# Performance work log

Hardware: AMD Instinct MI355X
Metric: run time of the kernel (lower is better)

Reference implementation:

```python
import jax, jax.numpy as jnp
import numpy as np

B, C, H, W = 8, 256, 64, 64
NUM_HEADS = 4


def setup_inputs() -> dict:
    key = jax.random.key(0)
    ks = jax.random.split(key, 6)
    s = 0.02  # small init scale for 1x1 conv weights
    return {
        "x": jax.random.normal(ks[0], (B, C, H, W), jnp.float32),
        "cproj": jax.random.normal(ks[1], (B, C, H, W), jnp.float32),
        "wq": jax.random.normal(ks[2], (C, C), jnp.float32) * s,
        "bq": jnp.zeros((C,), jnp.float32),
        "wkv": jax.random.normal(ks[3], (2 * C, C), jnp.float32) * s,
        "bkv": jnp.zeros((2 * C,), jnp.float32),
        "wo": jax.random.normal(ks[4], (C, C), jnp.float32) * s,  # zero_module in torch; random here for a meaningful baseline
        "bo": jnp.zeros((C,), jnp.float32),
    }


def reference(x, cproj, wq, bq, wkv, bkv, wo, bo):
    Bb, Cc, Hh, Ww = x.shape
    N = Hh * Ww
    h = NUM_HEADS
    d = Cc // h
    scale = 1.0 / jnp.sqrt(jnp.sqrt(jnp.asarray(Cc, jnp.float32)))

    xf = x.reshape(Bb, Cc, N)
    cf = cproj.reshape(Bb, Cc, N)

    # 1x1 convs == channel matmuls
    Q = jnp.einsum('oc,bcn->bon', wq, xf) + bq[None, :, None]           # (B,C,N)
    KV = jnp.einsum('oc,bcn->bon', wkv, cf) + bkv[None, :, None]        # (B,2C,N)
    K, V = KV[:, :Cc], KV[:, Cc:]

    # softmax over channel-dim-within-head for q, over spatial N for k
    q = jax.nn.softmax(Q.reshape(Bb, h, d, N) * scale, axis=2).reshape(Bb, Cc, N)
    k = jax.nn.softmax(K.reshape(Bb, h, d, N), axis=3).reshape(Bb, Cc, N)

    # linear-attention: (B,C,C) context, then project back to N — note heads are mixed, per original bmm
    context = jnp.einsum('bcn,bdn->bcd', k, V)
    out = jnp.einsum('bcd,bdn->bcn', context, q)

    out = jnp.einsum('oc,bcn->bon', wo, out) + bo[None, :, None]
    return out.reshape(Bb, Cc, Hh, Ww)
```

## Files before the change

kernel.cpp:

```cpp
#include <hip/hip_runtime.h>

#define B_ 8
#define C_ 256
#define N_ 4096
#define NSPLIT 16

typedef float f32x4 __attribute__((ext_vector_type(4)));
typedef __bf16 bf16x8 __attribute__((ext_vector_type(8)));
typedef unsigned short u16x8 __attribute__((ext_vector_type(8)));
typedef unsigned short u16x4 __attribute__((ext_vector_type(4)));

__device__ __forceinline__ unsigned short f2bf(float f) {
  unsigned u = __float_as_uint(f);
  u += 0x7fff + ((u >> 16) & 1);
  return (unsigned short)(u >> 16);
}

__device__ __forceinline__ f32x4 mfma16(bf16x8 a, bf16x8 b, f32x4 c) {
  return __builtin_amdgcn_mfma_f32_16x16x32_bf16(a, b, c, 0, 0, 0);
}

typedef __attribute__((address_space(1))) const void* gvp;
typedef __attribute__((address_space(3))) void* lvp;
__device__ __forceinline__ void gld16(const void* g, void* l) {
  __builtin_amdgcn_global_load_lds((gvp)g, (lvp)l, 16, 0, 0);
}

template <int ROWS>
__device__ __forceinline__ void stage(unsigned short* lds, const unsigned short* g,
                                      int ld, int w, int lane) {
  const int r8 = lane >> 3;
  const int ce = ((lane & 7) ^ r8) << 3;
  const unsigned short* gp = g + (size_t)(w * (ROWS / 4) + r8) * ld + ce;
  unsigned short* lp = lds + w * (ROWS / 4) * 64;
#pragma unroll
  for (int i = 0; i < ROWS / 32; i++)
    gld16(gp + (size_t)(i * 8) * ld, lp + i * 512);
}

__device__ __forceinline__ bf16x8 frag(const unsigned short* lds, int row, int kc) {
  return *(const bf16x8*)(lds + row * 64 + ((kc ^ (row & 7)) << 3));
}

__device__ __forceinline__ void loadB(float4* pbv, const float* src, int ld,
                                      int n0, int kt, int w, int lane) {
  const int nf = lane & 15, kg = lane >> 4;
  const float* sp = src + (size_t)(kt * 64 + w * 16 + kg * 4) * ld + n0 + 4 * nf;
#pragma unroll
  for (int i = 0; i < 4; i++) pbv[i] = *(const float4*)(sp + (size_t)i * ld);
}
__device__ __forceinline__ void writeB(unsigned short* Bs, const float4* pbv,
                                       int w, int lane) {
  const int nf = lane & 15, kg = lane >> 4;
  const int k0 = w * 16 + kg * 4;
#pragma unroll
  for (int j = 0; j < 4; j++) {
    u16x4 o = (u16x4){f2bf(((const float*)&pbv[0])[j]), f2bf(((const float*)&pbv[1])[j]),
                      f2bf(((const float*)&pbv[2])[j]), f2bf(((const float*)&pbv[3])[j])};
    *(u16x4*)&Bs[(4 * nf + j) * 68 + k0] = o;
  }
}
__device__ __forceinline__ bf16x8 fragB(const unsigned short* Bs, int n, int k8) {
  union { u16x4 q[2]; bf16x8 b; } u;
  const unsigned short* p = Bs + n * 68 + k8 * 8;
  u.q[0] = *(const u16x4*)p;
  u.q[1] = *(const u16x4*)(p + 4);
  return u.b;
}

__device__ __forceinline__ bf16x8 fragC(const unsigned short* Ct, int n, int k8) {
  union { u16x4 q[2]; bf16x8 b; } u;
  const unsigned short* p = Ct + n * 268 + k8 * 8;
  u.q[0] = *(const u16x4*)p;
  u.q[1] = *(const u16x4*)(p + 4);
  return u.b;
}

__global__ __launch_bounds__(256) void castw(
    const float* __restrict__ wq, const float* __restrict__ wkv,
    const float* __restrict__ wo, unsigned short* __restrict__ wqb,
    unsigned short* __restrict__ wkvb, unsigned short* __restrict__ wob,
    float* __restrict__ Z) {
  int t = blockIdx.x * 256 + threadIdx.x;
  if (t < B_ * C_) Z[t] = 0.f;
  int i = t * 4;
  const float* src;
  unsigned short* dst;
  int off;
  if (i < 65536) { src = wq; dst = wqb; off = i; }
  else if (i < 196608) { src = wkv; dst = wkvb; off = i - 65536; }
  else { src = wo; dst = wob; off = i - 196608; }
  float4 v = *(const float4*)(src + off);
  *(u16x4*)(dst + off) = (u16x4){f2bf(v.x), f2bf(v.y), f2bf(v.z), f2bf(v.w)};
}

__device__ __forceinline__ void qproj_body(
    unsigned short* As, unsigned short* Bs, const unsigned short* __restrict__ wqb,
    const float* __restrict__ x, const float* __restrict__ bq,
    unsigned short* __restrict__ qT, int b, int n0, int m0b) {
  const int tid = threadIdx.x, lane = tid & 63, w = tid >> 6;
  const int m0w = (w >> 1) * 64;
  const int n0w = (w & 1) * 32;
  const int colL = lane & 15, kq = lane >> 4, quad = lane >> 4;
  const float* xb = x + (size_t)b * C_ * N_;

  f32x4 acc[4][2];
#pragma unroll
  for (int i = 0; i < 4; i++)
#pragma unroll
    for (int j = 0; j < 2; j++) acc[i][j] = (f32x4){0.f, 0.f, 0.f, 0.f};

  float4 pbv[4];
  loadB(pbv, xb, N_, n0, 0, w, lane);

  for (int kt = 0; kt < 4; kt++) {
    writeB(Bs, pbv, w, lane);
    stage<128>(As, wqb + (size_t)m0b * C_ + kt * 64, C_, w, lane);
    __syncthreads();
    if (kt < 3) loadB(pbv, xb, N_, n0, kt + 1, w, lane);
#pragma unroll
    for (int ks = 0; ks < 2; ks++) {
      bf16x8 af[4], bf[2];
#pragma unroll
      for (int mt = 0; mt < 4; mt++) af[mt] = frag(As, m0w + mt * 16 + colL, ks * 4 + kq);
#pragma unroll
      for (int nt = 0; nt < 2; nt++) bf[nt] = fragB(Bs, n0w + nt * 16 + colL, ks * 4 + kq);
#pragma unroll
      for (int mt = 0; mt < 4; mt++)
#pragma unroll
        for (int nt = 0; nt < 2; nt++) acc[mt][nt] = mfma16(af[mt], bf[nt], acc[mt][nt]);
    }
    __syncthreads();
  }

#pragma unroll
  for (int nt = 0; nt < 2; nt++) {
    float v[16];
    float mx = -1e30f;
#pragma unroll
    for (int mt = 0; mt < 4; mt++)
#pragma unroll
      for (int r = 0; r < 4; r++) {
        int m = m0b + m0w + mt * 16 + quad * 4 + r;
        float val = (acc[mt][nt][r] + bq[m]) * 0.25f;
        v[mt * 4 + r] = val;
        mx = fmaxf(mx, val);
      }
    mx = fmaxf(mx, __shfl_xor(mx, 16));
    mx = fmaxf(mx, __shfl_xor(mx, 32));
    float s = 0.f;
#pragma unroll
    for (int j = 0; j < 16; j++) { v[j] = __expf(v[j] - mx); s += v[j]; }
    s += __shfl_xor(s, 16);
    s += __shfl_xor(s, 32);
    float inv = 1.0f / s;
    const int n = n0 + n0w + nt * 16 + colL;
    unsigned short* qb = qT + ((size_t)b * N_ + n) * C_ + m0b + m0w;
#pragma unroll
    for (int mt = 0; mt < 4; mt++) {
      u16x4 o = (u16x4){f2bf(v[mt * 4 + 0] * inv), f2bf(v[mt * 4 + 1] * inv),
                        f2bf(v[mt * 4 + 2] * inv), f2bf(v[mt * 4 + 3] * inv)};
      *(u16x4*)(qb + mt * 16 + quad * 4) = o;
    }
  }
}

__device__ __forceinline__ void kvproj_body(
    unsigned short* As, unsigned short* Bs, const unsigned short* __restrict__ wkvb,
    const float* __restrict__ cp, const float* __restrict__ bkv,
    float* __restrict__ Kf, unsigned short* __restrict__ Vb,
    float* __restrict__ Z, int b, int n0, int m0b) {
  const int tid = threadIdx.x, lane = tid & 63, w = tid >> 6;
  const int m0w = w * 32;
  const int colL = lane & 15, kq = lane >> 4, quad = lane >> 4;
  const float* cpb = cp + (size_t)b * C_ * N_;

  f32x4 acc[2][4];
#pragma unroll
  for (int i = 0; i < 2; i++)
#pragma unroll
    for (int j = 0; j < 4; j++) acc[i][j] = (f32x4){0.f, 0.f, 0.f, 0.f};

  float4 pbv[4];
  loadB(pbv, cpb, N_, n0, 0, w, lane);

  for (int kt = 0; kt < 4; kt++) {
    writeB(Bs, pbv, w, lane);
    stage<128>(As, wkvb + (size_t)m0b * C_ + kt * 64, C_, w, lane);
    __syncthreads();
    if (kt < 3) loadB(pbv, cpb, N_, n0, kt + 1, w, lane);
#pragma unroll
    for (int ks = 0; ks < 2; ks++) {
      bf16x8 bf[4];
#pragma unroll
      for (int nt = 0; nt < 4; nt++) bf[nt] = fragB(Bs, nt * 16 + colL, ks * 4 + kq);
#pragma unroll
      for (int mt = 0; mt < 2; mt++) {
        bf16x8 af = frag(As, m0w + mt * 16 + colL, ks * 4 + kq);
#pragma unroll
        for (int nt = 0; nt < 4; nt++) acc[mt][nt] = mfma16(af, bf[nt], acc[mt][nt]);
      }
    }
    __syncthreads();
  }

#pragma unroll
  for (int mt = 0; mt < 2; mt++)
#pragma unroll
    for (int r = 0; r < 4; r++) {
      int m = m0b + m0w + mt * 16 + quad * 4 + r;
      float bias = bkv[m];
      if (m < C_) {
        float* kr = Kf + ((size_t)b * C_ + m) * N_ + n0;
        float es = 0.f;
#pragma unroll
        for (int nt = 0; nt < 4; nt++) {
          float vv = acc[mt][nt][r] + bias;
          kr[nt * 16 + colL] = vv;
          es += __expf(vv);
        }
        es += __shfl_xor(es, 1);
        es += __shfl_xor(es, 2);
        es += __shfl_xor(es, 4);
        es += __shfl_xor(es, 8);
        if ((lane & 15) == 0) atomicAdd(&Z[b * C_ + m], es);
      } else {
        unsigned short* vr = Vb + ((size_t)b * C_ + m - C_) * N_ + n0;
#pragma unroll
        for (int nt = 0; nt < 4; nt++) vr[nt * 16 + colL] = f2bf(acc[mt][nt][r] + bias);
      }
    }
}

__global__ __launch_bounds__(256) void qkvproj(
    const unsigned short* __restrict__ wqb, const unsigned short* __restrict__ wkvb,
    const float* __restrict__ x, const float* __restrict__ cp,
    const float* __restrict__ bq, const float* __restrict__ bkv,
    unsigned short* __restrict__ qT, float* __restrict__ Kf,
    unsigned short* __restrict__ Vb, float* __restrict__ Z) {
  __shared__ __align__(16) unsigned short As[128 * 64];
  __shared__ __align__(16) unsigned short Bs[64 * 68];
  const int b = blockIdx.z, n0 = blockIdx.x * 64;
  if (blockIdx.y < 2)
    qproj_body(As, Bs, wqb, x, bq, qT, b, n0, blockIdx.y * 128);
  else
    kvproj_body(As, Bs, wkvb, cp, bkv, Kf, Vb, Z, b, n0, (blockIdx.y - 2) * 128);
}

__global__ __launch_bounds__(256) void ctx_part(
    const float* __restrict__ Kf, const float* __restrict__ Z,
    const unsigned short* __restrict__ Vb, float* __restrict__ ctxp) {
  __shared__ __align__(16) unsigned short As[128 * 64];
  __shared__ __align__(16) unsigned short Bs[64 * 64];
  const int z = blockIdx.z, b = z >> 4, s = z & 15;
  const int m0 = blockIdx.y * 128, n0 = blockIdx.x * 64;
  const int tid = threadIdx.x, lane = tid & 63, w = tid >> 6;
  const int m0w = (w & 1) * 64, n0w = (w >> 1) * 32;
  const int colL = lane & 15, kq = lane >> 4, quad = lane >> 4;
  const int kbeg = s * (N_ / NSPLIT);

  const int arow = tid >> 1, ahalf = tid & 1;
  const float* akf = Kf + ((size_t)b * C_ + m0 + arow) * N_ + kbeg + ahalf * 32;
  const float invz = 1.0f / Z[b * C_ + m0 + arow];
  const unsigned short* Bg = Vb + ((size_t)b * C_ + n0) * N_ + kbeg;

  f32x4 acc[4][2];
#pragma unroll
  for (int i = 0; i < 4; i++)
#pragma unroll
    for (int j = 0; j < 2; j++) acc[i][j] = (f32x4){0.f, 0.f, 0.f, 0.f};

  for (int kt = 0; kt < (N_ / NSPLIT) / 64; kt++) {
    stage<64>(Bs, Bg + kt * 64, N_, w, lane);
#pragma unroll
    for (int j = 0; j < 4; j++) {
      float4 a0 = *(const float4*)(akf + kt * 64 + j * 8);
      float4 a1 = *(const float4*)(akf + kt * 64 + j * 8 + 4);
      const int c8 = ahalf * 4 + j;
      u16x8 o = (u16x8){f2bf(__expf(a0.x) * invz), f2bf(__expf(a0.y) * invz),
                        f2bf(__expf(a0.z) * invz), f2bf(__expf(a0.w) * invz),
                        f2bf(__expf(a1.x) * invz), f2bf(__expf(a1.y) * invz),
                        f2bf(__expf(a1.z) * invz), f2bf(__expf(a1.w) * invz)};
      *(u16x8*)&As[arow * 64 + ((c8 ^ (arow & 7)) << 3)] = o;
    }
    __syncthreads();
#pragma unroll
    for (int ks = 0; ks < 2; ks++) {
      bf16x8 af[4], bf[2];
#pragma unroll
      for (int mt = 0; mt < 4; mt++) af[mt] = frag(As, m0w + mt * 16 + colL, ks * 4 + kq);
#pragma unroll
      for (int nt = 0; nt < 2; nt++) bf[nt] = frag(Bs, n0w + nt * 16 + colL, ks * 4 + kq);
#pragma unroll
      for (int mt = 0; mt < 4; mt++)
#pragma unroll
        for (int nt = 0; nt < 2; nt++) acc[mt][nt] = mfma16(af[mt], bf[nt], acc[mt][nt]);
    }
    __syncthreads();
  }

  float* outp = ctxp + ((size_t)s * B_ + b) * C_ * C_;
#pragma unroll
  for (int mt = 0; mt < 4; mt++)
#pragma unroll
    for (int nt = 0; nt < 2; nt++)
#pragma unroll
      for (int r = 0; r < 4; r++) {
        int m = m0 + m0w + mt * 16 + quad * 4 + r;
        int n = n0 + n0w + nt * 16 + colL;
        outp[(size_t)m * C_ + n] = acc[mt][nt][r];
      }
}

__global__ __launch_bounds__(256) void ctxoproj(
    const float* __restrict__ ctxp, const unsigned short* __restrict__ wob,
    unsigned short* __restrict__ ctx2) {
  __shared__ __align__(16) unsigned short AsW[4 * 64 * 64];
  __shared__ __align__(16) unsigned short Ct[32 * 268];
  const int b = blockIdx.z, o0 = blockIdx.y * 64, d0 = blockIdx.x * 32;
  const int tid = threadIdx.x, lane = tid & 63, w = tid >> 6;
  const int colL = lane & 15, kq = lane >> 4, quad = lane >> 4;

#pragma unroll
  for (int ck = 0; ck < 4; ck++)
    stage<64>(AsW + ck * 4096, wob + (size_t)o0 * C_ + ck * 64, C_, w, lane);

  const int q = tid & 7, cl = tid >> 3;
  const float* pb = ctxp + ((size_t)b * C_ + cl) * C_ + d0 + q * 4;
#pragma unroll 2
  for (int p = 0; p < 8; p++) {
    f32x4 s4 = (f32x4){0.f, 0.f, 0.f, 0.f};
    const float* pp = pb + (size_t)p * 32 * C_;
#pragma unroll
    for (int s = 0; s < NSPLIT; s++) {
      float4 v = *(const float4*)(pp + (size_t)s * B_ * C_ * C_);
      s4[0] += v.x; s4[1] += v.y; s4[2] += v.z; s4[3] += v.w;
    }
    const int c = p * 32 + cl;
#pragma unroll
    for (int j = 0; j < 4; j++) Ct[(q * 4 + j) * 268 + c] = f2bf(s4[j]);
  }
  __syncthreads();

  f32x4 acc2[2];
  acc2[0] = (f32x4){0.f, 0.f, 0.f, 0.f};
  acc2[1] = (f32x4){0.f, 0.f, 0.f, 0.f};
#pragma unroll
  for (int kt = 0; kt < 4; kt++)
#pragma unroll
    for (int ks = 0; ks < 2; ks++) {
      bf16x8 af = frag(AsW + kt * 4096, w * 16 + colL, ks * 4 + kq);
#pragma unroll
      for (int nt = 0; nt < 2; nt++) {
        bf16x8 bf = fragC(Ct, nt * 16 + colL, kt * 8 + ks * 4 + kq);
        acc2[nt] = mfma16(af, bf, acc2[nt]);
      }
    }
  unsigned short* ob = ctx2 + (size_t)b * C_ * C_;
#pragma unroll
  for (int nt = 0; nt < 2; nt++)
#pragma unroll
    for (int r = 0; r < 4; r++)
      ob[(size_t)(o0 + w * 16 + quad * 4 + r) * C_ + d0 + nt * 16 + colL] =
          f2bf(acc2[nt][r]);
}

__global__ __launch_bounds__(256) void outgemm(
    const unsigned short* __restrict__ ctx2, const unsigned short* __restrict__ qT,
    const float* __restrict__ bo, float* __restrict__ out) {
  __shared__ __align__(16) unsigned short As[128 * 64];
  __shared__ __align__(16) unsigned short Bs[64 * 64];
  const int b = blockIdx.z, n0 = blockIdx.x * 64, m0b = blockIdx.y * 128;
  const int tid = threadIdx.x, lane = tid & 63, w = tid >> 6;
  const int m0w = w * 32;
  const int colL = lane & 15, kq = lane >> 4, quad = lane >> 4;
  const unsigned short* Ag = ctx2 + (size_t)b * C_ * C_ + (size_t)m0b * C_;
  const unsigned short* Bg = qT + ((size_t)b * N_ + n0) * C_;

  f32x4 acc[2][4];
#pragma unroll
  for (int i = 0; i < 2; i++)
#pragma unroll
    for (int j = 0; j < 4; j++) acc[i][j] = (f32x4){0.f, 0.f, 0.f, 0.f};

  for (int kt = 0; kt < 4; kt++) {
    stage<128>(As, Ag + kt * 64, C_, w, lane);
    stage<64>(Bs, Bg + kt * 64, C_, w, lane);
    __syncthreads();
#pragma unroll
    for (int ks = 0; ks < 2; ks++) {
      bf16x8 af[2], bf[4];
#pragma unroll
      for (int mt = 0; mt < 2; mt++) af[mt] = frag(As, m0w + mt * 16 + colL, ks * 4 + kq);
#pragma unroll
      for (int nt = 0; nt < 4; nt++) bf[nt] = frag(Bs, nt * 16 + colL, ks * 4 + kq);
#pragma unroll
      for (int mt = 0; mt < 2; mt++)
#pragma unroll
        for (int nt = 0; nt < 4; nt++) acc[mt][nt] = mfma16(af[mt], bf[nt], acc[mt][nt]);
    }
    __syncthreads();
  }

  float* ob = out + (size_t)b * C_ * N_;
#pragma unroll
  for (int mt = 0; mt < 2; mt++)
#pragma unroll
    for (int r = 0; r < 4; r++) {
      int m = m0b + m0w + mt * 16 + quad * 4 + r;
      float bias = bo[m];
#pragma unroll
      for (int nt = 0; nt < 4; nt++) {
        int n = n0 + nt * 16 + colL;
        ob[(size_t)m * N_ + n] = acc[mt][nt][r] + bias;
      }
    }
}

extern "C" void kernel_launch(void* const* d_in, const int* in_sizes, int n_in,
                              void* d_out, int out_size, void* d_ws, size_t ws_size,
                              hipStream_t stream) {
  const float* x     = (const float*)d_in[0];
  const float* cproj = (const float*)d_in[1];
  const float* wq    = (const float*)d_in[2];
  const float* bq    = (const float*)d_in[3];
  const float* wkv   = (const float*)d_in[4];
  const float* bkv   = (const float*)d_in[5];
  const float* wo    = (const float*)d_in[6];
  const float* bo    = (const float*)d_in[7];
  float* out = (float*)d_out;

  unsigned short* qT    = (unsigned short*)d_ws;
  float*          Kf    = (float*)(qT + 8388608);
  unsigned short* Vb    = (unsigned short*)(Kf + 8388608);
  float*          ctxp  = (float*)(Vb + 8388608);
  unsigned short* wqb   = (unsigned short*)(ctxp + 8388608);
  unsigned short* wkvb  = wqb + 65536;
  unsigned short* wob   = wkvb + 131072;
  unsigned short* ctx2  = wob + 65536;
  float*          Zbuf  = (float*)(ctx2 + 524288);

  castw<<<256, 256, 0, stream>>>(wq, wkv, wo, wqb, wkvb, wob, Zbuf);
  qkvproj<<<dim3(64, 6, 8), 256, 0, stream>>>(wqb, wkvb, x, cproj, bq, bkv,
                                              qT, Kf, Vb, Zbuf);
  ctx_part<<<dim3(4, 2, 128), 256, 0, stream>>>(Kf, Zbuf, Vb, ctxp);
  ctxoproj<<<dim3(8, 4, 8), 256, 0, stream>>>(ctxp, wob, ctx2);
  outgemm<<<dim3(64, 2, 8), 256, 0, stream>>>(ctx2, qT, bo, out);
}
```

Measured before the change: 212.0 us.

## Pre-transpose inputs to bf16 and store exp(K) as bf16 for async staging

Adds a prep pass that casts x and cproj to bf16 and transposes them to N-major, so the projection GEMMs can stage both operands with direct global-to-LDS loads instead of register load, convert and scatter. The K projection now writes exp(K) as bf16 rather than fp32 logits, and the 1/Z normalisation moves to the ctx_part epilogue, which removes per-element exp and conversion from the context GEMM's inner loop. In exchange there is an extra full read and write of both inputs in the prep kernel and more workspace. The bf16 rounding of exp values before normalisation may change accuracy slightly.

```diff
diff --git a/kernel.cpp b/kernel.cpp
--- a/kernel.cpp
+++ b/kernel.cpp
@@ -42,32 +42,6 @@
   return *(const bf16x8*)(lds + row * 64 + ((kc ^ (row & 7)) << 3));
 }
 
-__device__ __forceinline__ void loadB(float4* pbv, const float* src, int ld,
-                                      int n0, int kt, int w, int lane) {
-  const int nf = lane & 15, kg = lane >> 4;
-  const float* sp = src + (size_t)(kt * 64 + w * 16 + kg * 4) * ld + n0 + 4 * nf;
-#pragma unroll
-  for (int i = 0; i < 4; i++) pbv[i] = *(const float4*)(sp + (size_t)i * ld);
-}
-__device__ __forceinline__ void writeB(unsigned short* Bs, const float4* pbv,
-                                       int w, int lane) {
-  const int nf = lane & 15, kg = lane >> 4;
-  const int k0 = w * 16 + kg * 4;
-#pragma unroll
-  for (int j = 0; j < 4; j++) {
-    u16x4 o = (u16x4){f2bf(((const float*)&pbv[0])[j]), f2bf(((const float*)&pbv[1])[j]),
-                      f2bf(((const float*)&pbv[2])[j]), f2bf(((const float*)&pbv[3])[j])};
-    *(u16x4*)&Bs[(4 * nf + j) * 68 + k0] = o;
-  }
-}
-__device__ __forceinline__ bf16x8 fragB(const unsigned short* Bs, int n, int k8) {
-  union { u16x4 q[2]; bf16x8 b; } u;
-  const unsigned short* p = Bs + n * 68 + k8 * 8;
-  u.q[0] = *(const u16x4*)p;
-  u.q[1] = *(const u16x4*)(p + 4);
-  return u.b;
-}
-
 __device__ __forceinline__ bf16x8 fragC(const unsigned short* Ct, int n, int k8) {
   union { u16x4 q[2]; bf16x8 b; } u;
   const unsigned short* p = Ct + n * 268 + k8 * 8;
@@ -76,33 +50,62 @@
   return u.b;
 }
 
-__global__ __launch_bounds__(256) void castw(
+__global__ __launch_bounds__(256) void prep(
+    const float* __restrict__ x, const float* __restrict__ cp,
     const float* __restrict__ wq, const float* __restrict__ wkv,
-    const float* __restrict__ wo, unsigned short* __restrict__ wqb,
+    const float* __restrict__ wo, unsigned short* __restrict__ xT,
+    unsigned short* __restrict__ cpT, unsigned short* __restrict__ wqb,
     unsigned short* __restrict__ wkvb, unsigned short* __restrict__ wob,
     float* __restrict__ Z) {
-  int t = blockIdx.x * 256 + threadIdx.x;
-  if (t < B_ * C_) Z[t] = 0.f;
-  int i = t * 4;
-  const float* src;
-  unsigned short* dst;
-  int off;
-  if (i < 65536) { src = wq; dst = wqb; off = i; }
-  else if (i < 196608) { src = wkv; dst = wkvb; off = i - 65536; }
-  else { src = wo; dst = wob; off = i - 196608; }
-  float4 v = *(const float4*)(src + off);
-  *(u16x4*)(dst + off) = (u16x4){f2bf(v.x), f2bf(v.y), f2bf(v.z), f2bf(v.w)};
+  const int bid = blockIdx.x, tid = threadIdx.x;
+  if (bid < 4096) {
+    const int ct = bid & 3, nt = (bid >> 2) & 63, b = (bid >> 8) & 7, s = bid >> 11;
+    const float* src = (s ? cp : x) + (size_t)b * C_ * N_;
+    unsigned short* dst = (s ? cpT : xT) + (size_t)b * N_ * C_;
+    const int n0 = nt * 64, c0 = ct * 64;
+    __shared__ unsigned short t[64][68];
+    const int c = tid >> 2, nq = (tid & 3) * 16;
+    const float* sp = src + (size_t)(c0 + c) * N_ + n0 + nq;
+#pragma unroll
+    for (int j = 0; j < 4; j++) {
+      float4 v = *(const float4*)(sp + j * 4);
+      *(u16x4*)&t[c][nq + j * 4] = (u16x4){f2bf(v.x), f2bf(v.y), f2bf(v.z), f2bf(v.w)};
+    }
+    __syncthreads();
+    const int n = tid >> 2, cq = (tid & 3) * 16;
+    union { unsigned short s16[16]; u16x8 v8[2]; } o;
+#pragma unroll
+    for (int j = 0; j < 16; j++) o.s16[j] = t[cq + j][n];
+    unsigned short* dp = dst + (size_t)(n0 + n) * C_ + c0 + cq;
+    *(u16x8*)dp = o.v8[0];
+    *(u16x8*)(dp + 8) = o.v8[1];
+  } else {
+    if (bid == 4096) {
+#pragma unroll
+      for (int j = 0; j < 8; j++) Z[tid * 8 + j] = 0.f;
+    }
+    int i = ((bid - 4096) * 256 + tid) * 4;
+    const float* src;
+    unsigned short* dst;
+    int off;
+    if (i < 65536) { src = wq; dst = wqb; off = i; }
+    else if (i < 196608) { src = wkv; dst = wkvb; off = i - 65536; }
+    else { src = wo; dst = wob; off = i - 196608; }
+    float4 v = *(const float4*)(src + off);
+    *(u16x4*)(dst + off) = (u16x4){f2bf(v.x), f2bf(v.y), f2bf(v.z), f2bf(v.w)};
+  }
 }
 
 __device__ __forceinline__ void qproj_body(
     unsigned short* As, unsigned short* Bs, const unsigned short* __restrict__ wqb,
-    const float* __restrict__ x, const float* __restrict__ bq,
+    const unsigned short* __restrict__ xT, const float* __restrict__ bq,
     unsigned short* __restrict__ qT, int b, int n0, int m0b) {
   const int tid = threadIdx.x, lane = tid & 63, w = tid >> 6;
   const int m0w = (w >> 1) * 64;
   const int n0w = (w & 1) * 32;
   const int colL = lane & 15, kq = lane >> 4, quad = lane >> 4;
-  const float* xb = x + (size_t)b * C_ * N_;
+  const unsigned short* Ag = wqb + (size_t)m0b * C_;
+  const unsigned short* Bg = xT + ((size_t)b * N_ + n0) * C_;
 
   f32x4 acc[4][2];
 #pragma unroll
@@ -110,21 +113,17 @@
 #pragma unroll
     for (int j = 0; j < 2; j++) acc[i][j] = (f32x4){0.f, 0.f, 0.f, 0.f};
 
-  float4 pbv[4];
-  loadB(pbv, xb, N_, n0, 0, w, lane);
-
   for (int kt = 0; kt < 4; kt++) {
-    writeB(Bs, pbv, w, lane);
-    stage<128>(As, wqb + (size_t)m0b * C_ + kt * 64, C_, w, lane);
-    __syncthreads();
-    if (kt < 3) loadB(pbv, xb, N_, n0, kt + 1, w, lane);
+    stage<128>(As, Ag + kt * 64, C_, w, lane);
+    stage<64>(Bs, Bg + kt * 64, C_, w, lane);
+    __syncthreads();
 #pragma unroll
     for (int ks = 0; ks < 2; ks++) {
       bf16x8 af[4], bf[2];
 #pragma unroll
       for (int mt = 0; mt < 4; mt++) af[mt] = frag(As, m0w + mt * 16 + colL, ks * 4 + kq);
 #pragma unroll
-      for (int nt = 0; nt < 2; nt++) bf[nt] = fragB(Bs, n0w + nt * 16 + colL, ks * 4 + kq);
+      for (int nt = 0; nt < 2; nt++) bf[nt] = frag(Bs, n0w + nt * 16 + colL, ks * 4 + kq);
 #pragma unroll
       for (int mt = 0; mt < 4; mt++)
 #pragma unroll
@@ -167,13 +166,14 @@
 
 __device__ __forceinline__ void kvproj_body(
     unsigned short* As, unsigned short* Bs, const unsigned short* __restrict__ wkvb,
-    const float* __restrict__ cp, const float* __restrict__ bkv,
-    float* __restrict__ Kf, unsigned short* __restrict__ Vb,
+    const unsigned short* __restrict__ cpT, const float* __restrict__ bkv,
+    unsigned short* __restrict__ Eb, unsigned short* __restrict__ Vb,
     float* __restrict__ Z, int b, int n0, int m0b) {
   const int tid = threadIdx.x, lane = tid & 63, w = tid >> 6;
   const int m0w = w * 32;
   const int colL = lane & 15, kq = lane >> 4, quad = lane >> 4;
-  const float* cpb = cp + (size_t)b * C_ * N_;
+  const unsigned short* Ag = wkvb + (size_t)m0b * C_;
+  const unsigned short* Bg = cpT + ((size_t)b * N_ + n0) * C_;
 
   f32x4 acc[2][4];
 #pragma unroll
@@ -181,19 +181,15 @@
 #pragma unroll
     for (int j = 0; j < 4; j++) acc[i][j] = (f32x4){0.f, 0.f, 0.f, 0.f};
 
-  float4 pbv[4];
-  loadB(pbv, cpb, N_, n0, 0, w, lane);
-
   for (int kt = 0; kt < 4; kt++) {
-    writeB(Bs, pbv, w, lane);
-    stage<128>(As, wkvb + (size_t)m0b * C_ + kt * 64, C_, w, lane);
-    __syncthreads();
-    if (kt < 3) loadB(pbv, cpb, N_, n0, kt + 1, w, lane);
+    stage<128>(As, Ag + kt * 64, C_, w, lane);
+    stage<64>(Bs, Bg + kt * 64, C_, w, lane);
+    __syncthreads();
 #pragma unroll
     for (int ks = 0; ks < 2; ks++) {
       bf16x8 bf[4];
 #pragma unroll
-      for (int nt = 0; nt < 4; nt++) bf[nt] = fragB(Bs, nt * 16 + colL, ks * 4 + kq);
+      for (int nt = 0; nt < 4; nt++) bf[nt] = frag(Bs, nt * 16 + colL, ks * 4 + kq);
 #pragma unroll
       for (int mt = 0; mt < 2; mt++) {
         bf16x8 af = frag(As, m0w + mt * 16 + colL, ks * 4 + kq);
@@ -211,13 +207,13 @@
       int m = m0b + m0w + mt * 16 + quad * 4 + r;
       float bias = bkv[m];
       if (m < C_) {
-        float* kr = Kf + ((size_t)b * C_ + m) * N_ + n0;
+        unsigned short* er = Eb + ((size_t)b * C_ + m) * N_ + n0;
         float es = 0.f;
 #pragma unroll
         for (int nt = 0; nt < 4; nt++) {
-          float vv = acc[mt][nt][r] + bias;
-          kr[nt * 16 + colL] = vv;
-          es += __expf(vv);
+          float e = __expf(acc[mt][nt][r] + bias);
+          er[nt * 16 + colL] = f2bf(e);
+          es += e;
         }
         es += __shfl_xor(es, 1);
         es += __shfl_xor(es, 2);
@@ -234,21 +230,21 @@
 
 __global__ __launch_bounds__(256) void qkvproj(
     const unsigned short* __restrict__ wqb, const unsigned short* __restrict__ wkvb,
-    const float* __restrict__ x, const float* __restrict__ cp,
+    const unsigned short* __restrict__ xT, const unsigned short* __restrict__ cpT,
     const float* __restrict__ bq, const float* __restrict__ bkv,
-    unsigned short* __restrict__ qT, float* __restrict__ Kf,
+    unsigned short* __restrict__ qT, unsigned short* __restrict__ Eb,
     unsigned short* __restrict__ Vb, float* __restrict__ Z) {
   __shared__ __align__(16) unsigned short As[128 * 64];
-  __shared__ __align__(16) unsigned short Bs[64 * 68];
+  __shared__ __align__(16) unsigned short Bs[64 * 64];
   const int b = blockIdx.z, n0 = blockIdx.x * 64;
   if (blockIdx.y < 2)
-    qproj_body(As, Bs, wqb, x, bq, qT, b, n0, blockIdx.y * 128);
+    qproj_body(As, Bs, wqb, xT, bq, qT, b, n0, blockIdx.y * 128);
   else
-    kvproj_body(As, Bs, wkvb, cp, bkv, Kf, Vb, Z, b, n0, (blockIdx.y - 2) * 128);
+    kvproj_body(As, Bs, wkvb, cpT, bkv, Eb, Vb, Z, b, n0, (blockIdx.y - 2) * 128);
 }
 
 __global__ __launch_bounds__(256) void ctx_part(
-    const float* __restrict__ Kf, const float* __restrict__ Z,
+    const unsigned short* __restrict__ Eb, const float* __restrict__ Z,
     const unsigned short* __restrict__ Vb, float* __restrict__ ctxp) {
   __shared__ __align__(16) unsigned short As[128 * 64];
   __shared__ __align__(16) unsigned short Bs[64 * 64];
@@ -257,13 +253,10 @@
   const int tid = threadIdx.x, lane = tid & 63, w = tid >> 6;
   const int m0w = (w & 1) * 64, n0w = (w >> 1) * 32;
   const int colL = lane & 15, kq = lane >> 4, quad = lane >> 4;
+  const unsigned short* Ag = Eb + ((size_t)b * C_ + m0) * N_;
+  const unsigned short* Bg = Vb + ((size_t)b * C_ + n0) * N_;
   const int kbeg = s * (N_ / NSPLIT);
 
-  const int arow = tid >> 1, ahalf = tid & 1;
-  const float* akf = Kf + ((size_t)b * C_ + m0 + arow) * N_ + kbeg + ahalf * 32;
-  const float invz = 1.0f / Z[b * C_ + m0 + arow];
-  const unsigned short* Bg = Vb + ((size_t)b * C_ + n0) * N_ + kbeg;
-
   f32x4 acc[4][2];
 #pragma unroll
   for (int i = 0; i < 4; i++)
@@ -271,18 +264,8 @@
     for (int j = 0; j < 2; j++) acc[i][j] = (f32x4){0.f, 0.f, 0.f, 0.f};
 
   for (int kt = 0; kt < (N_ / NSPLIT) / 64; kt++) {
-    stage<64>(Bs, Bg + kt * 64, N_, w, lane);
-#pragma unroll
-    for (int j = 0; j < 4; j++) {
-      float4 a0 = *(const float4*)(akf + kt * 64 + j * 8);
-      float4 a1 = *(const float4*)(akf + kt * 64 + j * 8 + 4);
-      const int c8 = ahalf * 4 + j;
-      u16x8 o = (u16x8){f2bf(__expf(a0.x) * invz), f2bf(__expf(a0.y) * invz),
-                        f2bf(__expf(a0.z) * invz), f2bf(__expf(a0.w) * invz),
-                        f2bf(__expf(a1.x) * invz), f2bf(__expf(a1.y) * invz),
-                        f2bf(__expf(a1.z) * invz), f2bf(__expf(a1.w) * invz)};
-      *(u16x8*)&As[arow * 64 + ((c8 ^ (arow & 7)) << 3)] = o;
-    }
+    stage<128>(As, Ag + kbeg + kt * 64, N_, w, lane);
+    stage<64>(Bs, Bg + kbeg + kt * 64, N_, w, lane);
     __syncthreads();
 #pragma unroll
     for (int ks = 0; ks < 2; ks++) {
@@ -300,16 +283,19 @@
   }
 
   float* outp = ctxp + ((size_t)s * B_ + b) * C_ * C_;
+  const float* Zb = Z + b * C_;
 #pragma unroll
   for (int mt = 0; mt < 4; mt++)
 #pragma unroll
-    for (int nt = 0; nt < 2; nt++)
-#pragma unroll
-      for (int r = 0; r < 4; r++) {
-        int m = m0 + m0w + mt * 16 + quad * 4 + r;
+    for (int r = 0; r < 4; r++) {
+      int m = m0 + m0w + mt * 16 + quad * 4 + r;
+      float iz = 1.0f / Zb[m];
+#pragma unroll
+      for (int nt = 0; nt < 2; nt++) {
         int n = n0 + n0w + nt * 16 + colL;
-        outp[(size_t)m * C_ + n] = acc[mt][nt][r];
-      }
+        outp[(size_t)m * C_ + n] = acc[mt][nt][r] * iz;
+      }
+    }
 }
 
 __global__ __launch_bounds__(256) void ctxoproj(
@@ -431,19 +417,21 @@
   float* out = (float*)d_out;
 
   unsigned short* qT    = (unsigned short*)d_ws;
-  float*          Kf    = (float*)(qT + 8388608);
-  unsigned short* Vb    = (unsigned short*)(Kf + 8388608);
-  float*          ctxp  = (float*)(Vb + 8388608);
+  unsigned short* Eb    = qT + 8388608;
+  unsigned short* Vb    = Eb + 8388608;
+  unsigned short* xT    = Vb + 8388608;
+  unsigned short* cpT   = xT + 8388608;
+  float*          ctxp  = (float*)(cpT + 8388608);
   unsigned short* wqb   = (unsigned short*)(ctxp + 8388608);
   unsigned short* wkvb  = wqb + 65536;
   unsigned short* wob   = wkvb + 131072;
   unsigned short* ctx2  = wob + 65536;
   float*          Zbuf  = (float*)(ctx2 + 524288);
 
-  castw<<<256, 256, 0, stream>>>(wq, wkv, wo, wqb, wkvb, wob, Zbuf);
-  qkvproj<<<dim3(64, 6, 8), 256, 0, stream>>>(wqb, wkvb, x, cproj, bq, bkv,
-                                              qT, Kf, Vb, Zbuf);
-  ctx_part<<<dim3(4, 2, 128), 256, 0, stream>>>(Kf, Zbuf, Vb, ctxp);
+  prep<<<4352, 256, 0, stream>>>(x, cproj, wq, wkv, wo, xT, cpT, wqb, wkvb, wob, Zbuf);
+  qkvproj<<<dim3(64, 6, 8), 256, 0, stream>>>(wqb, wkvb, xT, cpT, bq, bkv,
+                                              qT, Eb, Vb, Zbuf);
+  ctx_part<<<dim3(4, 2, 128), 256, 0, stream>>>(Eb, Zbuf, Vb, ctxp);
   ctxoproj<<<dim3(8, 4, 8), 256, 0, stream>>>(ctxp, wob, ctx2);
   outgemm<<<dim3(64, 2, 8), 256, 0, stream>>>(ctx2, qT, bo, out);
 }
```

After: 210.8 us. No clear change (-0.6%).
